# Kernel optimization log

Measured on AMD Instinct MI355X. Metric: run time of the kernel, lower is better.

The kernel has to match this reference:

```python
import jax, jax.numpy as jnp
import numpy as np

EPS = 1e-6
NEG = -1e9
RES_RATIO = 1.0  # res_ratio init arg
MAKE_SYM = True


def _ln(x, g, b):
    m = jnp.mean(x, axis=-1, keepdims=True)
    v = jnp.mean((x - m) ** 2, axis=-1, keepdims=True)
    return (x - m) * jax.lax.rsqrt(v + EPS) * g + b


def _sim(q, k, W1q, W1k, b1, W2, b2):
    # NN(concat([q,k])) with first dense split into query/key halves:
    # relu(q@W1q + k@W1k + b1) @ W2 + b2  -> avoids materializing the 2d concat.
    qa = q @ W1q  # [b,n,sq,h]
    kb = k @ W1k  # [b,n,sk,h]
    h1 = jax.nn.relu(qa[:, :, :, None, :] + kb[:, :, None, :, :] + b1)  # [b,n,sq,sk,h]
    s = jnp.einsum('bnqkh,h->bnqk', h1, W2[:, 0]) + b2[0]
    if MAKE_SYM:
        qb = q @ W1k
        ka = k @ W1q
        h2 = jax.nn.relu(ka[:, :, None, :, :] + qb[:, :, :, None, :] + b1)
        s = s + jnp.einsum('bnqkh,h->bnqk', h2, W2[:, 0]) + b2[0]
    return s


def _attention(v, k, q, mask, Ww, bw, Wd, bd, W1q, W1k, b1, W2, b2):
    q = q @ Ww + bw
    k = k @ Ww + bw
    v = v @ Ww + bw
    logits = _sim(q, k, W1q, W1k, b1, W2, b2)
    if mask is not None:
        logits = logits + mask * NEG
    attn = jax.nn.softmax(logits, axis=-1)
    out = jnp.einsum('bnqk,bnkd->bnqd', attn, v)
    return out @ Wd + bd, attn


def setup_inputs() -> dict:
    key = jax.random.key(0)
    B, N, S, D, DFF, H = 4, 1, 256, 128, 512, 128
    ks = jax.random.split(key, 16)
    s = 0.02
    inp = {
        'x': jax.random.normal(ks[0], (B, N, S, D), jnp.float32),
        'enc_output': jax.random.normal(ks[1], (B, N, S, D), jnp.float32),
        'com_mask': jnp.zeros((B, N, S, S), jnp.float32),
        'dec_mask': jnp.zeros((B, N, S, S), jnp.float32),
        # shared pairwise-score MLP NN: Dense(H, relu) -> Dense(1)
        'W1q': jax.random.normal(ks[2], (D, H), jnp.float32) * s,
        'W1k': jax.random.normal(ks[3], (D, H), jnp.float32) * s,
        'b1': jnp.zeros((H,), jnp.float32),
        'W2': jax.random.normal(ks[4], (H, 1), jnp.float32) * s,
        'b2': jnp.zeros((1,), jnp.float32),
        # mha1 projections
        'Ww1': jax.random.normal(ks[5], (D, D), jnp.float32) * s,
        'bw1': jnp.zeros((D,), jnp.float32),
        'Wd1': jax.random.normal(ks[6], (D, D), jnp.float32) * s,
        'bd1': jnp.zeros((D,), jnp.float32),
        # mha2 projections
        'Ww2': jax.random.normal(ks[7], (D, D), jnp.float32) * s,
        'bw2': jnp.zeros((D,), jnp.float32),
        'Wd2': jax.random.normal(ks[8], (D, D), jnp.float32) * s,
        'bd2': jnp.zeros((D,), jnp.float32),
        # ffn
        'Wf1': jax.random.normal(ks[9], (D, DFF), jnp.float32) * s,
        'bf1': jnp.zeros((DFF,), jnp.float32),
        'Wf2': jax.random.normal(ks[10], (DFF, D), jnp.float32) * s,
        'bf2': jnp.zeros((D,), jnp.float32),
        # layernorms
        'ln1_g': jnp.ones((D,), jnp.float32), 'ln1_b': jnp.zeros((D,), jnp.float32),
        'ln2_g': jnp.ones((D,), jnp.float32), 'ln2_b': jnp.zeros((D,), jnp.float32),
        'ln3_g': jnp.ones((D,), jnp.float32), 'ln3_b': jnp.zeros((D,), jnp.float32),
    }
    return inp


def reference(x, enc_output, com_mask, dec_mask,
              W1q, W1k, b1, W2, b2,
              Ww1, bw1, Wd1, bd1,
              Ww2, bw2, Wd2, bd2,
              Wf1, bf1, Wf2, bf2,
              ln1_g, ln1_b, ln2_g, ln2_b, ln3_g, ln3_b):
    r = RES_RATIO
    # self-attention block (dropout inactive, eval mode)
    attn1, aw1 = _attention(x, x, x, com_mask, Ww1, bw1, Wd1, bd1, W1q, W1k, b1, W2, b2)
    out1 = _ln((2 - r) * attn1 + r * x, ln1_g, ln1_b)
    # cross-attention block
    attn2, aw2 = _attention(enc_output, enc_output, out1, dec_mask, Ww2, bw2, Wd2, bd2, W1q, W1k, b1, W2, b2)
    out2 = _ln((2 - r) * attn2 + r * out1, ln2_g, ln2_b)
    # ffn
    ffn = jax.nn.relu(out2 @ Wf1 + bf1) @ Wf2 + bf2
    out3 = _ln((2 - r) * ffn + r * out2, ln3_g, ln3_b)
    return out3
```

## Files before the change

### kernel.cpp

```cpp
#include <hip/hip_runtime.h>
#include <math.h>


#define LN_EPS 1e-6f
#define NEGV  (-1e9f)

constexpr int B = 4, S = 256, D = 128, H = 128, DFF = 512;
constexpr int R = B * S;
constexpr int SP = 132;

struct P {
    const float *x, *enc, *com_mask, *dec_mask;
    const float *W1q, *W1k, *b1, *W2;
    const float *Ww1, *bw1, *Wd1, *bd1;
    const float *Ww2, *bw2, *Wd2, *bd2;
    const float *Wf1, *bf1, *Wf2, *bf2;
    const float *ln1g, *ln1b, *ln2g, *ln2b, *ln3g, *ln3b;
    float *out;
    float *xw, *qa, *kb, *kv2w, *kb2, *ka2, *qa2, *qb2, *out1;
};

__global__ __launch_bounds__(512) void proj3_kernel(P p)
{
    const int g = blockIdx.y, tid = threadIdx.x;
    const int r0 = blockIdx.x * 8;
    __shared__ __align__(16) float Ash[8 * 128];
    __shared__ __align__(16) float Pw[8 * 128];
    __shared__ __align__(16) float Pp[2 * 8 * 128];

    const float* A    = g ? p.enc  : p.x;
    const float* Wp   = g ? p.Ww2  : p.Ww1;
    const float* bp   = g ? p.bw2  : p.bw1;
    float*       o_w  = g ? p.kv2w : p.xw;
    const float* Wsec = g ? p.W1k  : p.W1q;
    const float* bsec = g ? nullptr: p.b1;
    float*       o_s  = g ? p.kb2  : p.qa;
    const float* Wthr = g ? p.W1q  : p.W1k;
    float*       o_t  = g ? p.ka2  : p.kb;

    if (tid < 256)
        ((float4*)Ash)[tid] = ((const float4*)(A + (size_t)r0 * 128))[tid];
    __syncthreads();

    {
        const int kh = tid >> 8, unit = tid & 255, lr = unit >> 5, c4 = unit & 31;
        const float4* W4 = (const float4*)Wp;
        float4 acc = (kh == 0) ? ((const float4*)bp)[c4] : make_float4(0.f, 0.f, 0.f, 0.f);
        const int k0 = kh * 64;
        #pragma unroll 8
        for (int k = 0; k < 64; ++k) {
            const float a = Ash[lr * 128 + k0 + k];
            const float4 w = W4[(k0 + k) * 32 + c4];
            acc.x = fmaf(a, w.x, acc.x); acc.y = fmaf(a, w.y, acc.y);
            acc.z = fmaf(a, w.z, acc.z); acc.w = fmaf(a, w.w, acc.w);
        }
        ((float4*)Pp)[kh * 256 + unit] = acc;
    }
    __syncthreads();
    if (tid < 256) {
        const int lr = tid >> 5, c4 = tid & 31;
        const float4 a = ((const float4*)Pp)[tid];
        const float4 bq = ((const float4*)Pp)[256 + tid];
        const float4 w = make_float4(a.x + bq.x, a.y + bq.y, a.z + bq.z, a.w + bq.w);
        ((float4*)Pw)[tid] = w;
        ((float4*)o_w)[(size_t)(r0 + lr) * 32 + c4] = w;
    }
    __syncthreads();

    {
        const int which = tid >> 8, unit = tid & 255, lr = unit >> 5, c4 = unit & 31;
        const float* W = which ? Wthr : Wsec;
        const float* bb = which ? nullptr : bsec;
        float* o = which ? o_t : o_s;
        const float4* W4 = (const float4*)W;
        float4 acc = bb ? ((const float4*)bb)[c4] : make_float4(0.f, 0.f, 0.f, 0.f);
        #pragma unroll 8
        for (int k = 0; k < 128; ++k) {
            const float a = Pw[lr * 128 + k];
            const float4 w = W4[k * 32 + c4];
            acc.x = fmaf(a, w.x, acc.x); acc.y = fmaf(a, w.y, acc.y);
            acc.z = fmaf(a, w.z, acc.z); acc.w = fmaf(a, w.w, acc.w);
        }
        ((float4*)o)[(size_t)(r0 + lr) * 32 + c4] = acc;
    }
}

#define SC8(ACC, O1, X1, O2, X2)                                               \
    ACC = fmaf(fmaxf((O1).x + (X1).x, 0.f), w.x, ACC);                         \
    ACC = fmaf(fmaxf((O1).y + (X1).y, 0.f), w.y, ACC);                         \
    ACC = fmaf(fmaxf((O1).z + (X1).z, 0.f), w.z, ACC);                         \
    ACC = fmaf(fmaxf((O1).w + (X1).w, 0.f), w.w, ACC);                         \
    ACC = fmaf(fmaxf((O2).x + (X2).x, 0.f), w.x, ACC);                         \
    ACC = fmaf(fmaxf((O2).y + (X2).y, 0.f), w.y, ACC);                         \
    ACC = fmaf(fmaxf((O2).z + (X2).z, 0.f), w.z, ACC);                         \
    ACC = fmaf(fmaxf((O2).w + (X2).w, 0.f), w.w, ACC);

template<bool FIRST>
__global__ __launch_bounds__(512) void fused_attn_kernel(P p)
{
    __shared__ __align__(16) float smem[18432];
    float* s8   = smem;
    float* rowS = smem + 1024;

    const int tid = threadIdx.x;
    const int r0 = blockIdx.x * 4, b = r0 >> 8, bS = b * S;

    const float* O1g  = FIRST ? p.qa  : p.qa2;
    const float* O2g  = FIRST ? p.kb  : p.qb2;
    const float* S1g  = FIRST ? p.kb  : p.kb2;
    const float* S2g  = FIRST ? p.qa  : p.ka2;
    const float* mask = FIRST ? p.com_mask : p.dec_mask;
    const float* V    = FIRST ? p.xw : p.kv2w;
    const float* Wd   = FIRST ? p.Wd1 : p.Wd2;
    const float* bd   = FIRST ? p.bd1 : p.bd2;
    const float* res  = FIRST ? p.x : p.out1;
    const float* lg   = FIRST ? p.ln1g : p.ln2g;
    const float* lb   = FIRST ? p.ln1b : p.ln2b;

    {
        float* stg1 = smem + 1536;
        float* stg2 = smem + 9984;
        const int hh = tid & 7, unit = tid >> 3, kk = unit & 31, rg = unit >> 5;
        const int rA = r0 + 2 * rg, rB = rA + 1;

        float4 o1A[4], o1B[4], o2A[4], o2B[4], w2r[4];
        #pragma unroll
        for (int j = 0; j < 4; ++j) {
            const int h = hh * 4 + 32 * j;
            o1A[j] = *(const float4*)(O1g + (size_t)rA * H + h);
            o1B[j] = *(const float4*)(O1g + (size_t)rB * H + h);
            o2A[j] = *(const float4*)(O2g + (size_t)rA * H + h);
            o2B[j] = *(const float4*)(O2g + (size_t)rB * H + h);
            w2r[j] = *(const float4*)(p.W2 + h);
        }

        for (int kt = 0; kt < 4; ++kt) {
            #pragma unroll
            for (int t = 0; t < 8; ++t) {
                const int fi = tid + t * 512;
                const int arr = fi >> 11, row = (fi >> 5) & 63, cf = (fi & 31) * 4;
                const float* gp = (arr ? S2g : S1g) + (size_t)(bS + kt * 64 + row) * H + cf;
                float* dp = (arr ? stg2 : stg1) + row * SP + cf;
                *(float4*)dp = *(const float4*)gp;
            }
            __syncthreads();

            const float* s1a = stg1 + kk * SP;
            const float* s1b = stg1 + (kk + 32) * SP;
            const float* s2a = stg2 + kk * SP;
            const float* s2b = stg2 + (kk + 32) * SP;
            float aAa = 0.f, aAb = 0.f, aBa = 0.f, aBb = 0.f;
            #pragma unroll
            for (int j = 0; j < 4; ++j) {
                const int h = hh * 4 + 32 * j;
                const float4 w = w2r[j];
                const float4 x1a = *(const float4*)(s1a + h);
                const float4 x1b = *(const float4*)(s1b + h);
                const float4 x2a = *(const float4*)(s2a + h);
                const float4 x2b = *(const float4*)(s2b + h);
                SC8(aAa, o1A[j], x1a, o2A[j], x2a)
                SC8(aAb, o1A[j], x1b, o2A[j], x2b)
                SC8(aBa, o1B[j], x1a, o2B[j], x2a)
                SC8(aBb, o1B[j], x1b, o2B[j], x2b)
            }
            #pragma unroll
            for (int o = 1; o < 8; o <<= 1) {
                aAa += __shfl_xor(aAa, o, 8);
                aAb += __shfl_xor(aAb, o, 8);
                aBa += __shfl_xor(aBa, o, 8);
                aBb += __shfl_xor(aBb, o, 8);
            }
            if (hh == 0) {
                const int kb0 = kt * 64;
                s8[(2 * rg)     * 256 + kb0 + kk]      = aAa;
                s8[(2 * rg)     * 256 + kb0 + kk + 32] = aAb;
                s8[(2 * rg + 1) * 256 + kb0 + kk]      = aBa;
                s8[(2 * rg + 1) * 256 + kb0 + kk + 32] = aBb;
            }
            __syncthreads();
        }
    }

    for (int i = tid; i < 1024; i += 512) {
        const int r = i >> 8, k = i & 255;
        s8[i] += mask[(size_t)(r0 + r) * S + k] * NEGV;
    }
    __syncthreads();

    {
        const int g = tid >> 6, c = tid & 63;
        if (g < 4) {
            float* rowp = s8 + g * 256;
            float m = -INFINITY;
            #pragma unroll
            for (int k = c; k < 256; k += 64) m = fmaxf(m, rowp[k]);
            for (int o = 32; o; o >>= 1) m = fmaxf(m, __shfl_xor(m, o, 64));
            float s = 0.f;
            #pragma unroll
            for (int k = c; k < 256; k += 64) { const float e = __expf(rowp[k] - m); rowp[k] = e; s += e; }
            for (int o = 32; o; o >>= 1) s += __shfl_xor(s, o, 64);
            const float rinv = 1.f / s;
            #pragma unroll
            for (int k = c; k < 256; k += 64) rowp[k] *= rinv;
        }
    }
    __syncthreads();

    float* avp = smem + 1536;
    float* aoS = smem + 3584;
    float* pp  = smem + 4096;

    {
        const int r = tid >> 7, t = tid & 127, kq = t >> 5, c4 = t & 31;
        const float4* V4 = (const float4*)(V + (size_t)bS * D);
        const float* sp = s8 + r * 256 + kq * 64;
        float4 acc = make_float4(0.f, 0.f, 0.f, 0.f);
        #pragma unroll 8
        for (int k = 0; k < 64; ++k) {
            const float a = sp[k];
            const float4 v = V4[(kq * 64 + k) * 32 + c4];
            acc.x = fmaf(a, v.x, acc.x); acc.y = fmaf(a, v.y, acc.y);
            acc.z = fmaf(a, v.z, acc.z); acc.w = fmaf(a, v.w, acc.w);
        }
        ((float4*)avp)[(r * 4 + kq) * 32 + c4] = acc;
    }
    __syncthreads();
    if (tid < 128) {
        const int r = tid >> 5, c4 = tid & 31;
        float4 s0 = ((const float4*)avp)[(r * 4 + 0) * 32 + c4];
        const float4 s1 = ((const float4*)avp)[(r * 4 + 1) * 32 + c4];
        const float4 s2 = ((const float4*)avp)[(r * 4 + 2) * 32 + c4];
        const float4 s3 = ((const float4*)avp)[(r * 4 + 3) * 32 + c4];
        s0.x += s1.x + s2.x + s3.x; s0.y += s1.y + s2.y + s3.y;
        s0.z += s1.z + s2.z + s3.z; s0.w += s1.w + s2.w + s3.w;
        ((float4*)aoS)[r * 32 + c4] = s0;
    }
    __syncthreads();

    {
        const int kq = tid >> 7, unit = tid & 127, r = unit >> 5, c4 = unit & 31;
        const float4* W4 = (const float4*)Wd;
        const float* ap = aoS + r * 128 + kq * 32;
        float4 acc = make_float4(0.f, 0.f, 0.f, 0.f);
        #pragma unroll 8
        for (int k = 0; k < 32; ++k) {
            const float a = ap[k];
            const float4 w = W4[(kq * 32 + k) * 32 + c4];
            acc.x = fmaf(a, w.x, acc.x); acc.y = fmaf(a, w.y, acc.y);
            acc.z = fmaf(a, w.z, acc.z); acc.w = fmaf(a, w.w, acc.w);
        }
        ((float4*)pp)[kq * 128 + unit] = acc;
    }
    __syncthreads();

    if (tid < 128) {
        const int r = tid >> 5, c4 = tid & 31;
        const float4 p0 = ((const float4*)pp)[tid];
        const float4 p1 = ((const float4*)pp)[128 + tid];
        const float4 p2 = ((const float4*)pp)[256 + tid];
        const float4 p3 = ((const float4*)pp)[384 + tid];
        const float4 bv0 = ((const float4*)bd)[c4];
        const float4 r4 = ((const float4*)(res + (size_t)(r0 + r) * 128))[c4];
        const float x0 = p0.x + p1.x + p2.x + p3.x + bv0.x + r4.x;
        const float x1 = p0.y + p1.y + p2.y + p3.y + bv0.y + r4.y;
        const float x2 = p0.z + p1.z + p2.z + p3.z + bv0.z + r4.z;
        const float x3 = p0.w + p1.w + p2.w + p3.w + bv0.w + r4.w;
        float s  = x0 + x1 + x2 + x3;
        float s2 = x0 * x0 + x1 * x1 + x2 * x2 + x3 * x3;
        for (int o = 16; o; o >>= 1) { s += __shfl_xor(s, o, 32); s2 += __shfl_xor(s2, o, 32); }
        const float m = s * (1.f / 128), var = s2 * (1.f / 128) - m * m;
        const float rs = rsqrtf(var + LN_EPS);
        const float4 gv = ((const float4*)lg)[c4], bv = ((const float4*)lb)[c4];
        float4 o4;
        o4.x = (x0 - m) * rs * gv.x + bv.x; o4.y = (x1 - m) * rs * gv.y + bv.y;
        o4.z = (x2 - m) * rs * gv.z + bv.z; o4.w = (x3 - m) * rs * gv.w + bv.w;
        ((float4*)rowS)[r * 32 + c4] = o4;
        if (FIRST) ((float4*)p.out1)[(size_t)(r0 + r) * 32 + c4] = o4;
    }
    __syncthreads();

    if (FIRST) {
        float* qpp  = smem + 6144;
        float* q2wS = smem + 8192;
        float* qp2  = smem + 8704;
        {
            const int kq = tid >> 7, unit = tid & 127, r = unit >> 5, c4 = unit & 31;
            const float4* W4 = (const float4*)p.Ww2;
            const float* ap = rowS + r * 128 + kq * 32;
            float4 acc = make_float4(0.f, 0.f, 0.f, 0.f);
            #pragma unroll 8
            for (int k = 0; k < 32; ++k) {
                const float a = ap[k];
                const float4 w = W4[(kq * 32 + k) * 32 + c4];
                acc.x = fmaf(a, w.x, acc.x); acc.y = fmaf(a, w.y, acc.y);
                acc.z = fmaf(a, w.z, acc.z); acc.w = fmaf(a, w.w, acc.w);
            }
            ((float4*)qpp)[kq * 128 + unit] = acc;
        }
        __syncthreads();
        if (tid < 128) {
            const int c4 = tid & 31;
            const float4 p0 = ((const float4*)qpp)[tid];
            const float4 p1 = ((const float4*)qpp)[128 + tid];
            const float4 p2 = ((const float4*)qpp)[256 + tid];
            const float4 p3 = ((const float4*)qpp)[384 + tid];
            const float4 bw = ((const float4*)p.bw2)[c4];
            ((float4*)q2wS)[tid] = make_float4(p0.x + p1.x + p2.x + p3.x + bw.x,
                                               p0.y + p1.y + p2.y + p3.y + bw.y,
                                               p0.z + p1.z + p2.z + p3.z + bw.z,
                                               p0.w + p1.w + p2.w + p3.w + bw.w);
        }
        __syncthreads();
        {
            const int which = tid >> 8, sub = tid & 255;
            const int kh = sub >> 7, unit2 = sub & 127;
            const float4* W4 = (const float4*)(which ? p.W1k : p.W1q);
            const int r = unit2 >> 5, c4 = unit2 & 31;
            const float* ap = q2wS + r * 128 + kh * 64;
            float4 acc = make_float4(0.f, 0.f, 0.f, 0.f);
            #pragma unroll 8
            for (int k = 0; k < 64; ++k) {
                const float a = ap[k];
                const float4 w = W4[(kh * 64 + k) * 32 + c4];
                acc.x = fmaf(a, w.x, acc.x); acc.y = fmaf(a, w.y, acc.y);
                acc.z = fmaf(a, w.z, acc.z); acc.w = fmaf(a, w.w, acc.w);
            }
            ((float4*)qp2)[(which * 2 + kh) * 128 + unit2] = acc;
        }
        __syncthreads();
        if (tid < 256) {
            const int which = tid >> 7, unit2 = tid & 127;
            const int r = unit2 >> 5, c4 = unit2 & 31;
            const float4 p0 = ((const float4*)qp2)[(which * 2 + 0) * 128 + unit2];
            const float4 p1 = ((const float4*)qp2)[(which * 2 + 1) * 128 + unit2];
            const float4 b1v = ((const float4*)p.b1)[c4];
            float* oq = which ? p.qb2 : p.qa2;
            ((float4*)oq)[(size_t)(r0 + r) * 32 + c4] =
                make_float4(p0.x + p1.x + b1v.x, p0.y + p1.y + b1v.y,
                            p0.z + p1.z + b1v.z, p0.w + p1.w + b1v.w);
        }
    } else {
        float* hidP = smem + 1536;
        float* part = smem + 9984;
        {
            const int c = tid & 127, kh = tid >> 7;
            const float4* Wf1_4 = (const float4*)p.Wf1;
            float4 a0 = make_float4(0.f,0.f,0.f,0.f), a1 = a0, a2 = a0, a3 = a0;
            const int kbase = kh * 32;
            #pragma unroll 8
            for (int k = 0; k < 32; ++k) {
                const int kk = kbase + k;
                const float4 w = Wf1_4[kk * 128 + c];
                const float s0 = rowS[kk],       s1 = rowS[128 + kk];
                const float s2 = rowS[256 + kk], s3 = rowS[384 + kk];
                a0.x=fmaf(s0,w.x,a0.x); a0.y=fmaf(s0,w.y,a0.y); a0.z=fmaf(s0,w.z,a0.z); a0.w=fmaf(s0,w.w,a0.w);
                a1.x=fmaf(s1,w.x,a1.x); a1.y=fmaf(s1,w.y,a1.y); a1.z=fmaf(s1,w.z,a1.z); a1.w=fmaf(s1,w.w,a1.w);
                a2.x=fmaf(s2,w.x,a2.x); a2.y=fmaf(s2,w.y,a2.y); a2.z=fmaf(s2,w.z,a2.z); a2.w=fmaf(s2,w.w,a2.w);
                a3.x=fmaf(s3,w.x,a3.x); a3.y=fmaf(s3,w.y,a3.y); a3.z=fmaf(s3,w.z,a3.z); a3.w=fmaf(s3,w.w,a3.w);
            }
            float4* h4 = (float4*)hidP;
            const int base = kh * 512;
            h4[base + 0*128 + c] = a0; h4[base + 1*128 + c] = a1;
            h4[base + 2*128 + c] = a2; h4[base + 3*128 + c] = a3;
        }
        __syncthreads();
        for (int i = tid; i < 2048; i += 512) {
            hidP[i] = fmaxf(hidP[i] + hidP[2048 + i] + hidP[4096 + i] + hidP[6144 + i]
                            + p.bf1[i & 511], 0.f);
        }
        __syncthreads();
        {
            const int c4f = tid & 31, kg = tid >> 5;
            const float4* Wf2_4 = (const float4*)p.Wf2;
            float4 a0 = make_float4(0.f,0.f,0.f,0.f), a1 = a0, a2 = a0, a3 = a0;
            const int kbase = kg * 32;
            const float* h0 = hidP + 0 * 512 + kbase;
            const float* h1 = hidP + 1 * 512 + kbase;
            const float* h2 = hidP + 2 * 512 + kbase;
            const float* h3 = hidP + 3 * 512 + kbase;
            #pragma unroll 8
            for (int k = 0; k < 32; ++k) {
                const float4 w = Wf2_4[(kbase + k) * 32 + c4f];
                const float s0 = h0[k], s1 = h1[k], s2 = h2[k], s3 = h3[k];
                a0.x=fmaf(s0,w.x,a0.x); a0.y=fmaf(s0,w.y,a0.y); a0.z=fmaf(s0,w.z,a0.z); a0.w=fmaf(s0,w.w,a0.w);
                a1.x=fmaf(s1,w.x,a1.x); a1.y=fmaf(s1,w.y,a1.y); a1.z=fmaf(s1,w.z,a1.z); a1.w=fmaf(s1,w.w,a1.w);
                a2.x=fmaf(s2,w.x,a2.x); a2.y=fmaf(s2,w.y,a2.y); a2.z=fmaf(s2,w.z,a2.z); a2.w=fmaf(s2,w.w,a2.w);
                a3.x=fmaf(s3,w.x,a3.x); a3.y=fmaf(s3,w.y,a3.y); a3.z=fmaf(s3,w.z,a3.z); a3.w=fmaf(s3,w.w,a3.w);
            }
            float4* p4 = (float4*)part;
            p4[kg * 128 + 0 * 32 + c4f] = a0; p4[kg * 128 + 1 * 32 + c4f] = a1;
            p4[kg * 128 + 2 * 32 + c4f] = a2; p4[kg * 128 + 3 * 32 + c4f] = a3;
        }
        __syncthreads();
        if (tid < 128) {
            const int r = tid >> 5, c4 = tid & 31;
            const float4* p4 = (const float4*)part;
            float4 sum = ((const float4*)p.bf2)[c4];
            #pragma unroll
            for (int kg = 0; kg < 16; ++kg) {
                const float4 v = p4[kg * 128 + r * 32 + c4];
                sum.x += v.x; sum.y += v.y; sum.z += v.z; sum.w += v.w;
            }
            const float4 r4 = ((const float4*)rowS)[r * 32 + c4];
            const float x0 = sum.x + r4.x, x1 = sum.y + r4.y;
            const float x2 = sum.z + r4.z, x3 = sum.w + r4.w;
            float s  = x0 + x1 + x2 + x3;
            float s2 = x0 * x0 + x1 * x1 + x2 * x2 + x3 * x3;
            for (int o = 16; o; o >>= 1) { s += __shfl_xor(s, o, 32); s2 += __shfl_xor(s2, o, 32); }
            const float m = s * (1.f / 128), var = s2 * (1.f / 128) - m * m;
            const float rs = rsqrtf(var + LN_EPS);
            const float4 gv = ((const float4*)p.ln3g)[c4], bv = ((const float4*)p.ln3b)[c4];
            float4 o4;
            o4.x = (x0 - m) * rs * gv.x + bv.x; o4.y = (x1 - m) * rs * gv.y + bv.y;
            o4.z = (x2 - m) * rs * gv.z + bv.z; o4.w = (x3 - m) * rs * gv.w + bv.w;
            ((float4*)p.out)[(size_t)(r0 + r) * 32 + c4] = o4;
        }
    }
}

extern "C" void kernel_launch(void* const* d_in, const int* in_sizes, int n_in,
                              void* d_out, int out_size, void* d_ws, size_t ws_size,
                              hipStream_t stream) {
    (void)in_sizes; (void)n_in; (void)out_size; (void)ws_size;
    P p;
    p.x        = (const float*)d_in[0];
    p.enc      = (const float*)d_in[1];
    p.com_mask = (const float*)d_in[2];
    p.dec_mask = (const float*)d_in[3];
    p.W1q = (const float*)d_in[4];
    p.W1k = (const float*)d_in[5];
    p.b1  = (const float*)d_in[6];
    p.W2  = (const float*)d_in[7];
    p.Ww1 = (const float*)d_in[9];
    p.bw1 = (const float*)d_in[10];
    p.Wd1 = (const float*)d_in[11];
    p.bd1 = (const float*)d_in[12];
    p.Ww2 = (const float*)d_in[13];
    p.bw2 = (const float*)d_in[14];
    p.Wd2 = (const float*)d_in[15];
    p.bd2 = (const float*)d_in[16];
    p.Wf1 = (const float*)d_in[17];
    p.bf1 = (const float*)d_in[18];
    p.Wf2 = (const float*)d_in[19];
    p.bf2 = (const float*)d_in[20];
    p.ln1g = (const float*)d_in[21];
    p.ln1b = (const float*)d_in[22];
    p.ln2g = (const float*)d_in[23];
    p.ln2b = (const float*)d_in[24];
    p.ln3g = (const float*)d_in[25];
    p.ln3b = (const float*)d_in[26];
    p.out  = (float*)d_out;

    float* ws = (float*)d_ws;
    const size_t RD = (size_t)R * D;
    p.xw    = ws;
    p.qa    = p.xw    + RD;
    p.kb    = p.qa    + RD;
    p.kv2w  = p.kb    + RD;
    p.kb2   = p.kv2w  + RD;
    p.ka2   = p.kb2   + RD;
    p.qa2   = p.ka2   + RD;
    p.qb2   = p.qa2   + RD;
    p.out1  = p.qb2   + RD;

    proj3_kernel<<<dim3(R / 8, 2), 512, 0, stream>>>(p);
    fused_attn_kernel<true><<<R / 4, 512, 0, stream>>>(p);
    fused_attn_kernel<false><<<R / 4, 512, 0, stream>>>(p);
}
```

Baseline: 174.1 us.

## Fuse projection and both attention stages into one persistent kernel with grid barrier

Merges the projection kernel and both attention kernels into a single 256-block kernel. A global atomic counter acts as a grid-wide barrier after the projection phase. Each block then runs self-attention and cross-attention back to back on the same 4 rows, keeping out1, qa2 and qb2 in shared memory instead of writing them to global memory. This removes two kernel launches and some global round trips, but adds a memset and a spin barrier that relies on all 256 blocks being co-resident.

```diff
diff --git a/kernel.cpp b/kernel.cpp
--- a/kernel.cpp
+++ b/kernel.cpp
@@ -8,6 +8,7 @@
 constexpr int B = 4, S = 256, D = 128, H = 128, DFF = 512;
 constexpr int R = B * S;
 constexpr int SP = 132;
+constexpr unsigned int NBLK = 256;
 
 struct P {
     const float *x, *enc, *com_mask, *dec_mask;
@@ -17,73 +18,9 @@
     const float *Wf1, *bf1, *Wf2, *bf2;
     const float *ln1g, *ln1b, *ln2g, *ln2b, *ln3g, *ln3b;
     float *out;
-    float *xw, *qa, *kb, *kv2w, *kb2, *ka2, *qa2, *qb2, *out1;
+    unsigned int *ctr;
+    float *xw, *qa, *kb, *kv2w, *kb2, *ka2;
 };
-
-__global__ __launch_bounds__(512) void proj3_kernel(P p)
-{
-    const int g = blockIdx.y, tid = threadIdx.x;
-    const int r0 = blockIdx.x * 8;
-    __shared__ __align__(16) float Ash[8 * 128];
-    __shared__ __align__(16) float Pw[8 * 128];
-    __shared__ __align__(16) float Pp[2 * 8 * 128];
-
-    const float* A    = g ? p.enc  : p.x;
-    const float* Wp   = g ? p.Ww2  : p.Ww1;
-    const float* bp   = g ? p.bw2  : p.bw1;
-    float*       o_w  = g ? p.kv2w : p.xw;
-    const float* Wsec = g ? p.W1k  : p.W1q;
-    const float* bsec = g ? nullptr: p.b1;
-    float*       o_s  = g ? p.kb2  : p.qa;
-    const float* Wthr = g ? p.W1q  : p.W1k;
-    float*       o_t  = g ? p.ka2  : p.kb;
-
-    if (tid < 256)
-        ((float4*)Ash)[tid] = ((const float4*)(A + (size_t)r0 * 128))[tid];
-    __syncthreads();
-
-    {
-        const int kh = tid >> 8, unit = tid & 255, lr = unit >> 5, c4 = unit & 31;
-        const float4* W4 = (const float4*)Wp;
-        float4 acc = (kh == 0) ? ((const float4*)bp)[c4] : make_float4(0.f, 0.f, 0.f, 0.f);
-        const int k0 = kh * 64;
-        #pragma unroll 8
-        for (int k = 0; k < 64; ++k) {
-            const float a = Ash[lr * 128 + k0 + k];
-            const float4 w = W4[(k0 + k) * 32 + c4];
-            acc.x = fmaf(a, w.x, acc.x); acc.y = fmaf(a, w.y, acc.y);
-            acc.z = fmaf(a, w.z, acc.z); acc.w = fmaf(a, w.w, acc.w);
-        }
-        ((float4*)Pp)[kh * 256 + unit] = acc;
-    }
-    __syncthreads();
-    if (tid < 256) {
-        const int lr = tid >> 5, c4 = tid & 31;
-        const float4 a = ((const float4*)Pp)[tid];
-        const float4 bq = ((const float4*)Pp)[256 + tid];
-        const float4 w = make_float4(a.x + bq.x, a.y + bq.y, a.z + bq.z, a.w + bq.w);
-        ((float4*)Pw)[tid] = w;
-        ((float4*)o_w)[(size_t)(r0 + lr) * 32 + c4] = w;
-    }
-    __syncthreads();
-
-    {
-        const int which = tid >> 8, unit = tid & 255, lr = unit >> 5, c4 = unit & 31;
-        const float* W = which ? Wthr : Wsec;
-        const float* bb = which ? nullptr : bsec;
-        float* o = which ? o_t : o_s;
-        const float4* W4 = (const float4*)W;
-        float4 acc = bb ? ((const float4*)bb)[c4] : make_float4(0.f, 0.f, 0.f, 0.f);
-        #pragma unroll 8
-        for (int k = 0; k < 128; ++k) {
-            const float a = Pw[lr * 128 + k];
-            const float4 w = W4[k * 32 + c4];
-            acc.x = fmaf(a, w.x, acc.x); acc.y = fmaf(a, w.y, acc.y);
-            acc.z = fmaf(a, w.z, acc.z); acc.w = fmaf(a, w.w, acc.w);
-        }
-        ((float4*)o)[(size_t)(r0 + lr) * 32 + c4] = acc;
-    }
-}
 
 #define SC8(ACC, O1, X1, O2, X2)                                               \
     ACC = fmaf(fmaxf((O1).x + (X1).x, 0.f), w.x, ACC);                         \
@@ -96,24 +33,20 @@
     ACC = fmaf(fmaxf((O2).w + (X2).w, 0.f), w.w, ACC);
 
 template<bool FIRST>
-__global__ __launch_bounds__(512) void fused_attn_kernel(P p)
+__device__ __forceinline__ void attn_stage(const P& p, float* smem,
+                                           int tid, int r0, int bS)
 {
-    __shared__ __align__(16) float smem[18432];
     float* s8   = smem;
     float* rowS = smem + 1024;
-
-    const int tid = threadIdx.x;
-    const int r0 = blockIdx.x * 4, b = r0 >> 8, bS = b * S;
-
-    const float* O1g  = FIRST ? p.qa  : p.qa2;
-    const float* O2g  = FIRST ? p.kb  : p.qb2;
-    const float* S1g  = FIRST ? p.kb  : p.kb2;
-    const float* S2g  = FIRST ? p.qa  : p.ka2;
+    float* qa2L = smem + 18432;
+    float* qb2L = smem + 18944;
+
+    const float* S1g  = FIRST ? p.kb : p.kb2;
+    const float* S2g  = FIRST ? p.qa : p.ka2;
     const float* mask = FIRST ? p.com_mask : p.dec_mask;
     const float* V    = FIRST ? p.xw : p.kv2w;
     const float* Wd   = FIRST ? p.Wd1 : p.Wd2;
     const float* bd   = FIRST ? p.bd1 : p.bd2;
-    const float* res  = FIRST ? p.x : p.out1;
     const float* lg   = FIRST ? p.ln1g : p.ln2g;
     const float* lb   = FIRST ? p.ln1b : p.ln2b;
 
@@ -127,12 +60,20 @@
         #pragma unroll
         for (int j = 0; j < 4; ++j) {
             const int h = hh * 4 + 32 * j;
-            o1A[j] = *(const float4*)(O1g + (size_t)rA * H + h);
-            o1B[j] = *(const float4*)(O1g + (size_t)rB * H + h);
-            o2A[j] = *(const float4*)(O2g + (size_t)rA * H + h);
-            o2B[j] = *(const float4*)(O2g + (size_t)rB * H + h);
+            if (FIRST) {
+                o1A[j] = *(const float4*)(p.qa + (size_t)rA * H + h);
+                o1B[j] = *(const float4*)(p.qa + (size_t)rB * H + h);
+                o2A[j] = *(const float4*)(p.kb + (size_t)rA * H + h);
+                o2B[j] = *(const float4*)(p.kb + (size_t)rB * H + h);
+            } else {
+                o1A[j] = *(const float4*)(qa2L + (2 * rg)     * H + h);
+                o1B[j] = *(const float4*)(qa2L + (2 * rg + 1) * H + h);
+                o2A[j] = *(const float4*)(qb2L + (2 * rg)     * H + h);
+                o2B[j] = *(const float4*)(qb2L + (2 * rg + 1) * H + h);
+            }
             w2r[j] = *(const float4*)(p.W2 + h);
         }
+        __syncthreads();
 
         for (int kt = 0; kt < 4; ++kt) {
             #pragma unroll
@@ -260,7 +201,9 @@
         const float4 p2 = ((const float4*)pp)[256 + tid];
         const float4 p3 = ((const float4*)pp)[384 + tid];
         const float4 bv0 = ((const float4*)bd)[c4];
-        const float4 r4 = ((const float4*)(res + (size_t)(r0 + r) * 128))[c4];
+        float4 r4;
+        if (FIRST) r4 = ((const float4*)(p.x + (size_t)(r0 + r) * 128))[c4];
+        else       r4 = ((const float4*)rowS)[r * 32 + c4];
         const float x0 = p0.x + p1.x + p2.x + p3.x + bv0.x + r4.x;
         const float x1 = p0.y + p1.y + p2.y + p3.y + bv0.y + r4.y;
         const float x2 = p0.z + p1.z + p2.z + p3.z + bv0.z + r4.z;
@@ -275,7 +218,6 @@
         o4.x = (x0 - m) * rs * gv.x + bv.x; o4.y = (x1 - m) * rs * gv.y + bv.y;
         o4.z = (x2 - m) * rs * gv.z + bv.z; o4.w = (x3 - m) * rs * gv.w + bv.w;
         ((float4*)rowS)[r * 32 + c4] = o4;
-        if (FIRST) ((float4*)p.out1)[(size_t)(r0 + r) * 32 + c4] = o4;
     }
     __syncthreads();
 
@@ -315,13 +257,13 @@
             const int which = tid >> 8, sub = tid & 255;
             const int kh = sub >> 7, unit2 = sub & 127;
             const float4* W4 = (const float4*)(which ? p.W1k : p.W1q);
-            const int r = unit2 >> 5, c4 = unit2 & 31;
+            const int r = unit2 >> 5;
             const float* ap = q2wS + r * 128 + kh * 64;
             float4 acc = make_float4(0.f, 0.f, 0.f, 0.f);
             #pragma unroll 8
             for (int k = 0; k < 64; ++k) {
                 const float a = ap[k];
-                const float4 w = W4[(kh * 64 + k) * 32 + c4];
+                const float4 w = W4[(kh * 64 + k) * 32 + (unit2 & 31)];
                 acc.x = fmaf(a, w.x, acc.x); acc.y = fmaf(a, w.y, acc.y);
                 acc.z = fmaf(a, w.z, acc.z); acc.w = fmaf(a, w.w, acc.w);
             }
@@ -330,15 +272,16 @@
         __syncthreads();
         if (tid < 256) {
             const int which = tid >> 7, unit2 = tid & 127;
-            const int r = unit2 >> 5, c4 = unit2 & 31;
+            const int c4 = unit2 & 31;
             const float4 p0 = ((const float4*)qp2)[(which * 2 + 0) * 128 + unit2];
             const float4 p1 = ((const float4*)qp2)[(which * 2 + 1) * 128 + unit2];
             const float4 b1v = ((const float4*)p.b1)[c4];
-            float* oq = which ? p.qb2 : p.qa2;
-            ((float4*)oq)[(size_t)(r0 + r) * 32 + c4] =
+            float* oq = which ? qb2L : qa2L;
+            ((float4*)oq)[unit2] =
                 make_float4(p0.x + p1.x + b1v.x, p0.y + p1.y + b1v.y,
                             p0.z + p1.z + b1v.z, p0.w + p1.w + b1v.w);
         }
+        __syncthreads();
     } else {
         float* hidP = smem + 1536;
         float* part = smem + 9984;
@@ -416,6 +359,90 @@
             ((float4*)p.out)[(size_t)(r0 + r) * 32 + c4] = o4;
         }
     }
+}
+
+__global__ __launch_bounds__(512) void mega_kernel(P p)
+{
+    __shared__ __align__(16) float smem[19456];
+    const int tid = threadIdx.x, bid = blockIdx.x;
+
+    {
+        const int g = bid >> 7;
+        const int r0p = (bid & 127) * 8;
+        float* Ash = smem + 1536;
+        float* Pw  = smem + 2560;
+        float* Pp  = smem + 3584;
+
+        const float* A    = g ? p.enc  : p.x;
+        const float* Wp   = g ? p.Ww2  : p.Ww1;
+        const float* bp   = g ? p.bw2  : p.bw1;
+        float*       o_w  = g ? p.kv2w : p.xw;
+        const float* Wsec = g ? p.W1k  : p.W1q;
+        const float* bsec = g ? nullptr: p.b1;
+        float*       o_s  = g ? p.kb2  : p.qa;
+        const float* Wthr = g ? p.W1q  : p.W1k;
+        float*       o_t  = g ? p.ka2  : p.kb;
+
+        if (tid < 256)
+            ((float4*)Ash)[tid] = ((const float4*)(A + (size_t)r0p * 128))[tid];
+        __syncthreads();
+
+        {
+            const int kh = tid >> 8, unit = tid & 255, lr = unit >> 5, c4 = unit & 31;
+            const float4* W4 = (const float4*)Wp;
+            float4 acc = (kh == 0) ? ((const float4*)bp)[c4] : make_float4(0.f, 0.f, 0.f, 0.f);
+            const int k0 = kh * 64;
+            #pragma unroll 8
+            for (int k = 0; k < 64; ++k) {
+                const float a = Ash[lr * 128 + k0 + k];
+                const float4 w = W4[(k0 + k) * 32 + c4];
+                acc.x = fmaf(a, w.x, acc.x); acc.y = fmaf(a, w.y, acc.y);
+                acc.z = fmaf(a, w.z, acc.z); acc.w = fmaf(a, w.w, acc.w);
+            }
+            ((float4*)Pp)[kh * 256 + unit] = acc;
+        }
+        __syncthreads();
+        if (tid < 256) {
+            const int lr = tid >> 5, c4 = tid & 31;
+            const float4 a = ((const float4*)Pp)[tid];
+            const float4 bq = ((const float4*)Pp)[256 + tid];
+            const float4 w = make_float4(a.x + bq.x, a.y + bq.y, a.z + bq.z, a.w + bq.w);
+            ((float4*)Pw)[tid] = w;
+            ((float4*)o_w)[(size_t)(r0p + lr) * 32 + c4] = w;
+        }
+        __syncthreads();
+        {
+            const int which = tid >> 8, unit = tid & 255, lr = unit >> 5, c4 = unit & 31;
+            const float* W = which ? Wthr : Wsec;
+            const float* bb = which ? nullptr : bsec;
+            float* o = which ? o_t : o_s;
+            const float4* W4 = (const float4*)W;
+            float4 acc = bb ? ((const float4*)bb)[c4] : make_float4(0.f, 0.f, 0.f, 0.f);
+            #pragma unroll 8
+            for (int k = 0; k < 128; ++k) {
+                const float a = Pw[lr * 128 + k];
+                const float4 w = W4[k * 32 + c4];
+                acc.x = fmaf(a, w.x, acc.x); acc.y = fmaf(a, w.y, acc.y);
+                acc.z = fmaf(a, w.z, acc.z); acc.w = fmaf(a, w.w, acc.w);
+            }
+            ((float4*)o)[(size_t)(r0p + lr) * 32 + c4] = acc;
+        }
+    }
+
+    __threadfence();
+    __syncthreads();
+    if (tid == 0) {
+        __hip_atomic_fetch_add(p.ctr, 1u, __ATOMIC_ACQ_REL, __HIP_MEMORY_SCOPE_AGENT);
+        while (__hip_atomic_load(p.ctr, __ATOMIC_ACQUIRE, __HIP_MEMORY_SCOPE_AGENT) < NBLK) {
+            __builtin_amdgcn_s_sleep(2);
+        }
+    }
+    __syncthreads();
+    __threadfence();
+
+    const int r0 = bid * 4, bS = (r0 >> 8) * S;
+    attn_stage<true >(p, smem, tid, r0, bS);
+    attn_stage<false>(p, smem, tid, r0, bS);
 }
 
 extern "C" void kernel_launch(void* const* d_in, const int* in_sizes, int n_in,
@@ -451,7 +478,8 @@
     p.ln3b = (const float*)d_in[26];
     p.out  = (float*)d_out;
 
-    float* ws = (float*)d_ws;
+    p.ctr = (unsigned int*)d_ws;
+    float* ws = (float*)d_ws + 64;
     const size_t RD = (size_t)R * D;
     p.xw    = ws;
     p.qa    = p.xw    + RD;
@@ -459,11 +487,7 @@
     p.kv2w  = p.kb    + RD;
     p.kb2   = p.kv2w  + RD;
     p.ka2   = p.kb2   + RD;
-    p.qa2   = p.ka2   + RD;
-    p.qb2   = p.qa2   + RD;
-    p.out1  = p.qb2   + RD;
-
-    proj3_kernel<<<dim3(R / 8, 2), 512, 0, stream>>>(p);
-    fused_attn_kernel<true><<<R / 4, 512, 0, stream>>>(p);
-    fused_attn_kernel<false><<<R / 4, 512, 0, stream>>>(p);
+
+    hipMemsetAsync(d_ws, 0, 256, stream);
+    mega_kernel<<<NBLK, 512, 0, stream>>>(p);
 }
```

Result: slower. 252.0 us (+44.7%).
